# Kernel tuning notes

Hardware: AMD Instinct MI355X
Metric: run time of the kernel (lower is better)

## Reference

```python
import jax, jax.numpy as jnp
import numpy as np

FOCAL_LENGTH = 1000.0
IMG_SIZE = 512.0
EPS = 1e-8


def setup_inputs() -> dict:
    key = jax.random.key(0)
    ks = jax.random.split(key, 11)
    B, J, V = 512, 24, 6890
    return {
        "pred_rotmat": jax.random.normal(ks[0], (B, J, 3, 3), jnp.float32),
        "pred_camera": jax.random.uniform(ks[1], (B, 3), jnp.float32, 0.2, 1.0),
        "pred_joints": jax.random.normal(ks[2], (B, J, 3), jnp.float32),
        "pred_vertices": jax.random.normal(ks[3], (B, V, 3), jnp.float32),
        "pred_betas": jax.random.normal(ks[4], (B, 10), jnp.float32),
        "gt_rotmat": jax.random.normal(ks[5], (B, J, 3, 3), jnp.float32),
        "gt_shape": jax.random.normal(ks[6], (B, 10), jnp.float32),
        "gt_keypoints_2d": jax.random.uniform(ks[7], (B, J, 3), jnp.float32),
        "gt_keypoints_3d": jax.random.uniform(ks[8], (B, J, 4), jnp.float32),
        "gt_vertices": jax.random.normal(ks[9], (B, V, 3), jnp.float32),
        "has_smpl": jax.random.randint(ks[10], (B,), 0, 2, jnp.int32),
    }


def _procrustes_align(S1, S2):
    # S1, S2: [B, N, 3] -> similarity transform of S1 onto S2 (batched closed-form Procrustes)
    S1 = jnp.swapaxes(S1, 1, 2)  # [B,3,N]
    S2 = jnp.swapaxes(S2, 1, 2)
    mu1 = jnp.mean(S1, axis=-1, keepdims=True)
    mu2 = jnp.mean(S2, axis=-1, keepdims=True)
    X1 = S1 - mu1
    X2 = S2 - mu2
    var1 = jnp.sum(X1 * X1, axis=(1, 2))  # [B]
    K = jnp.matmul(X1, jnp.swapaxes(X2, 1, 2)) + EPS  # [B,3,3]
    U, s, Vh = jnp.linalg.svd(K)
    Vt = Vh  # torch V^T == jax Vh
    sign = jnp.sign(jnp.linalg.det(jnp.matmul(U, Vt)))  # det(U @ V^T)
    Z = jnp.broadcast_to(jnp.eye(3, dtype=S1.dtype), K.shape)
    Z = Z.at[:, -1, -1].multiply(sign)
    R = jnp.matmul(jnp.swapaxes(Vh, 1, 2), jnp.matmul(Z, jnp.swapaxes(U, 1, 2)))
    scale = jnp.trace(jnp.matmul(R, K), axis1=1, axis2=2) / var1  # [B]
    t = mu2 - scale[:, None, None] * jnp.matmul(R, mu1)
    S1_hat = scale[:, None, None] * jnp.matmul(R, S1) + t
    return jnp.swapaxes(S1_hat, 1, 2), jnp.swapaxes(S2, 1, 2)


def reference(pred_rotmat, pred_camera, pred_joints, pred_vertices, pred_betas,
              gt_rotmat, gt_shape, gt_keypoints_2d, gt_keypoints_3d, gt_vertices,
              has_smpl):
    B = pred_joints.shape[0]
    f = jnp.float32(FOCAL_LENGTH)
    img = jnp.float32(IMG_SIZE)

    # --- perspective projection with identity rotation ---
    depth = 2.0 * f / (EPS + pred_camera[:, 0] * img)  # [B]
    translation = jnp.stack([pred_camera[:, 1], pred_camera[:, 2], depth], axis=-1)  # [B,3]
    pts = pred_joints + translation[:, None, :]  # [B,J,3]
    pred_kp2d = f * pts[..., :2] / pts[..., 2:3] + img / 2.0  # [B,J,2]

    # --- 2D keypoint loss (normalized by image size, confidence weighted L1) ---
    pred_kp2d_n = pred_kp2d / img
    gt_kp2d_n = gt_keypoints_2d[..., :2] / img
    conf2d = gt_keypoints_2d[..., 2:]
    loss_kp2d = jnp.mean(conf2d * jnp.abs(pred_kp2d_n - gt_kp2d_n))

    # --- 3D keypoint loss (pelvis-aligned, confidence weighted L1) ---
    conf3d = gt_keypoints_3d[..., 3:]
    gt3 = gt_keypoints_3d[..., :3]
    gt_pelvis = (gt3[:, 2:3] + gt3[:, 3:4]) / 2.0
    pr_pelvis = (pred_joints[:, 2:3] + pred_joints[:, 3:4]) / 2.0
    loss_kp3d = jnp.mean(conf3d * jnp.abs((pred_joints - pr_pelvis) - (gt3 - gt_pelvis)))

    # --- masked shape / SMPL parameter losses ---
    mask = (has_smpl > 0).astype(pred_vertices.dtype)  # [B]
    n_valid = jnp.sum(mask)
    V = pred_vertices.shape[1]
    loss_shape = jnp.sum(mask[:, None, None] * jnp.abs(pred_vertices - gt_vertices)) / (n_valid * V * 3 + EPS)
    loss_pose = jnp.sum(mask[:, None, None, None] * (pred_rotmat - gt_rotmat) ** 2) / (n_valid * 24 * 9 + EPS)
    loss_betas = jnp.sum(mask[:, None] * (pred_betas - gt_shape) ** 2) / (n_valid * 10 + EPS)

    # --- PA-MPJPE via batched 3x3 SVD Procrustes (eval-only in original: no grad) ---
    S1_hat, S2 = _procrustes_align(pred_joints, gt3)
    pa_mpjpe = jnp.mean(jnp.sqrt(jnp.sum((S1_hat - S2) ** 2, axis=-1)))

    total = (4.0 * loss_kp2d + 4.0 * loss_kp3d + loss_shape + loss_pose
             + 0.01 * loss_betas + jax.lax.stop_gradient(pa_mpjpe))
    return total
```

## Files before the change

### kernel.cpp

```cpp
#include <hip/hip_runtime.h>
#include <math.h>

#define EPSF   1e-8f
#define NV4    2645760
#define PER_B  20670
#define VBLK   2048

#define B_PROC   0
#define B_NV     8
#define B_BETA   10
#define B_KP2D   30
#define B_KP3D   78
#define B_POSE   126
#define B_VERT   558
#define NBLK     2606


__device__ __forceinline__ void block_sum_store(float v, double* dst) {
  #pragma unroll
  for (int off = 32; off > 0; off >>= 1) v += __shfl_down(v, off);
  __shared__ float red[4];
  const int lane = threadIdx.x & 63;
  const int wid  = threadIdx.x >> 6;
  if (lane == 0) red[wid] = v;
  __syncthreads();
  if (threadIdx.x == 0) *dst = (double)(red[0] + red[1] + red[2] + red[3]);
}

template<int P, int Q>
__device__ __forceinline__ void jrot(float A[3][3], float Vv[3][3]) {
  float apq = A[P][Q];
  if (fabsf(apq) < 1e-20f) return;
  float tau = (A[Q][Q] - A[P][P]) / (2.f * apq);
  float t   = copysignf(1.f, tau) / (fabsf(tau) + sqrtf(1.f + tau * tau));
  float c   = 1.f / sqrtf(1.f + t * t);
  float s   = t * c;
  float cP[3], cQ[3];
  #pragma unroll
  for (int k = 0; k < 3; ++k) { cP[k] = c*A[k][P] - s*A[k][Q]; cQ[k] = s*A[k][P] + c*A[k][Q]; }
  #pragma unroll
  for (int k = 0; k < 3; ++k) { A[k][P] = cP[k]; A[k][Q] = cQ[k]; }
  float rP[3], rQ[3];
  #pragma unroll
  for (int k = 0; k < 3; ++k) { rP[k] = c*A[P][k] - s*A[Q][k]; rQ[k] = s*A[P][k] + c*A[Q][k]; }
  #pragma unroll
  for (int k = 0; k < 3; ++k) { A[P][k] = rP[k]; A[Q][k] = rQ[k]; }
  #pragma unroll
  for (int k = 0; k < 3; ++k) {
    float vp = c*Vv[k][P] - s*Vv[k][Q];
    Vv[k][Q] = s*Vv[k][P] + c*Vv[k][Q];
    Vv[k][P] = vp;
  }
}

#define CSWAP(I, J)                                                        \
  if (lam[I] < lam[J]) {                                                   \
    float tl = lam[I]; lam[I] = lam[J]; lam[J] = tl;                       \
    _Pragma("unroll")                                                      \
    for (int r = 0; r < 3; ++r) {                                          \
      float tv = Vv[r][I]; Vv[r][I] = Vv[r][J]; Vv[r][J] = tv;             \
    }                                                                      \
  }

__device__ float procrustes_err(const float4* __restrict__ P4,
                                const float4* __restrict__ G4, int b) {
  const float4* Pr = P4 + b * 18;
  const float4* Gr = G4 + b * 24;

  float sx0=0,sx1=0,sx2=0, sy0=0,sy1=0,sy2=0, sxx=0;
  float Ku[3][3] = {{0,0,0},{0,0,0},{0,0,0}};
  #pragma unroll
  for (int g = 0; g < 6; ++g) {
    float4 p0 = Pr[g*3+0], p1 = Pr[g*3+1], p2 = Pr[g*3+2];
    float px[4][3] = {{p0.x,p0.y,p0.z},{p0.w,p1.x,p1.y},
                      {p1.z,p1.w,p2.x},{p2.y,p2.z,p2.w}};
    #pragma unroll
    for (int q = 0; q < 4; ++q) {
      float4 gg = Gr[g*4+q];
      float x0 = px[q][0], x1 = px[q][1], x2 = px[q][2];
      sx0 += x0; sx1 += x1; sx2 += x2;
      sy0 += gg.x; sy1 += gg.y; sy2 += gg.z;
      sxx += x0*x0 + x1*x1 + x2*x2;
      Ku[0][0]+=x0*gg.x; Ku[0][1]+=x0*gg.y; Ku[0][2]+=x0*gg.z;
      Ku[1][0]+=x1*gg.x; Ku[1][1]+=x1*gg.y; Ku[1][2]+=x1*gg.z;
      Ku[2][0]+=x2*gg.x; Ku[2][1]+=x2*gg.y; Ku[2][2]+=x2*gg.z;
    }
  }
  const float inv24 = 1.f / 24.f;
  float mu1x=sx0*inv24, mu1y=sx1*inv24, mu1z=sx2*inv24;
  float mu2x=sy0*inv24, mu2y=sy1*inv24, mu2z=sy2*inv24;
  float m1[3] = {mu1x, mu1y, mu1z};
  float m2[3] = {mu2x, mu2y, mu2z};
  float K[3][3];
  #pragma unroll
  for (int r = 0; r < 3; ++r)
    #pragma unroll
    for (int c = 0; c < 3; ++c)
      K[r][c] = Ku[r][c] - 24.f * m1[r] * m2[c] + EPSF;
  float var1 = sxx - 24.f * (mu1x*mu1x + mu1y*mu1y + mu1z*mu1z);

  float detK = K[0][0]*(K[1][1]*K[2][2]-K[1][2]*K[2][1])
             - K[0][1]*(K[1][0]*K[2][2]-K[1][2]*K[2][0])
             + K[0][2]*(K[1][0]*K[2][1]-K[1][1]*K[2][0]);
  float sgn = (detK > 0.f) ? 1.f : ((detK < 0.f) ? -1.f : 0.f);

  float A[3][3];
  #pragma unroll
  for (int r = 0; r < 3; ++r)
    #pragma unroll
    for (int c = 0; c < 3; ++c)
      A[r][c] = K[0][r]*K[0][c] + K[1][r]*K[1][c] + K[2][r]*K[2][c];

  float Vv[3][3] = {{1,0,0},{0,1,0},{0,0,1}};
  for (int sweep = 0; sweep < 8; ++sweep) {
    jrot<0,1>(A, Vv); jrot<0,2>(A, Vv); jrot<1,2>(A, Vv);
  }
  float lam[3] = {A[0][0], A[1][1], A[2][2]};
  CSWAP(0,1) CSWAP(0,2) CSWAP(1,2)

  float Rm[3][3] = {{0,0,0},{0,0,0},{0,0,0}};
  float zi[3] = {1.f, 1.f, sgn};
  float trRK = 0.f;
  #pragma unroll
  for (int i = 0; i < 3; ++i) {
    float v0 = Vv[0][i], v1 = Vv[1][i], v2 = Vv[2][i];
    float a0 = K[0][0]*v0 + K[0][1]*v1 + K[0][2]*v2;
    float a1 = K[1][0]*v0 + K[1][1]*v1 + K[1][2]*v2;
    float a2 = K[2][0]*v0 + K[2][1]*v1 + K[2][2]*v2;
    float si = sqrtf(a0*a0 + a1*a1 + a2*a2);
    float zs = zi[i] / fmaxf(si, 1e-20f);
    Rm[0][0]+=zs*v0*a0; Rm[0][1]+=zs*v0*a1; Rm[0][2]+=zs*v0*a2;
    Rm[1][0]+=zs*v1*a0; Rm[1][1]+=zs*v1*a1; Rm[1][2]+=zs*v1*a2;
    Rm[2][0]+=zs*v2*a0; Rm[2][1]+=zs*v2*a1; Rm[2][2]+=zs*v2*a2;
    trRK += zi[i] * si;
  }
  float scale = trRK / var1;
  float t0 = mu2x - scale*(Rm[0][0]*mu1x + Rm[0][1]*mu1y + Rm[0][2]*mu1z);
  float t1 = mu2y - scale*(Rm[1][0]*mu1x + Rm[1][1]*mu1y + Rm[1][2]*mu1z);
  float t2 = mu2z - scale*(Rm[2][0]*mu1x + Rm[2][1]*mu1y + Rm[2][2]*mu1z);

  float errsum = 0.f;
  #pragma unroll
  for (int g = 0; g < 6; ++g) {
    float4 p0 = Pr[g*3+0], p1 = Pr[g*3+1], p2 = Pr[g*3+2];
    float px[4][3] = {{p0.x,p0.y,p0.z},{p0.w,p1.x,p1.y},
                      {p1.z,p1.w,p2.x},{p2.y,p2.z,p2.w}};
    #pragma unroll
    for (int q = 0; q < 4; ++q) {
      float4 gg = Gr[g*4+q];
      float X = px[q][0], Y = px[q][1], Z = px[q][2];
      float q0 = scale*(Rm[0][0]*X + Rm[0][1]*Y + Rm[0][2]*Z) + t0;
      float q1 = scale*(Rm[1][0]*X + Rm[1][1]*Y + Rm[1][2]*Z) + t1;
      float q2 = scale*(Rm[2][0]*X + Rm[2][1]*Y + Rm[2][2]*Z) + t2;
      float d0 = q0 - gg.x, d1 = q1 - gg.y, d2 = q2 - gg.z;
      errsum += sqrtf(d0*d0 + d1*d1 + d2*d2);
    }
  }
  return errsum;
}

__global__ __launch_bounds__(256) void bmp_main(
    const float*  __restrict__ pred_rotmat, const float* __restrict__ pred_camera,
    const float*  __restrict__ pred_joints, const float4* __restrict__ pred_verts,
    const float*  __restrict__ pred_betas,  const float* __restrict__ gt_rotmat,
    const float*  __restrict__ gt_shape,    const float* __restrict__ gt_kp2d,
    const float*  __restrict__ gt_kp3d,     const float4* __restrict__ gt_verts,
    const int*    __restrict__ has_smpl,    double* __restrict__ ws) {
  const int bid = blockIdx.x;
  const int tid = threadIdx.x;

  if (bid >= B_VERT) {
    float acc = 0.f;
    for (int i = (bid - B_VERT) * 256 + tid; i < NV4; i += VBLK * 256) {
      float4 a = pred_verts[i];
      float4 b = gt_verts[i];
      int e  = i * 4;
      int b0 = e / PER_B;
      int b3 = (e + 3) / PER_B;
      if (b0 == b3) {
        if (has_smpl[b0] > 0)
          acc += fabsf(a.x-b.x) + fabsf(a.y-b.y) + fabsf(a.z-b.z) + fabsf(a.w-b.w);
      } else {
        float d[4] = {fabsf(a.x-b.x), fabsf(a.y-b.y), fabsf(a.z-b.z), fabsf(a.w-b.w)};
        #pragma unroll
        for (int c = 0; c < 4; ++c) {
          int bb = (e + c) / PER_B;
          if (has_smpl[bb] > 0) acc += d[c];
        }
      }
    }
    block_sum_store(acc, &ws[bid]);
    return;
  }

  if (bid >= B_POSE) {
    int idx = (bid - B_POSE) * 256 + tid;
    int b   = idx / 216;
    float m = (has_smpl[b] > 0) ? 1.f : 0.f;
    float d = pred_rotmat[idx] - gt_rotmat[idx];
    block_sum_store(m * d * d, &ws[bid]);
    return;
  }

  if (bid >= B_KP3D) {
    int idx = (bid - B_KP3D) * 256 + tid;
    int b = idx / 24, j = idx - (idx / 24) * 24;
    const float* PJ = pred_joints + b * 72;
    const float* G  = gt_kp3d + b * 96;
    float cf = G[j*4+3];
    float ssum = 0.f;
    #pragma unroll
    for (int c = 0; c < 3; ++c) {
      float prp = 0.5f * (PJ[2*3+c] + PJ[3*3+c]);
      float gtp = 0.5f * (G[2*4+c] + G[3*4+c]);
      ssum += fabsf((PJ[j*3+c] - prp) - (G[j*4+c] - gtp));
    }
    block_sum_store(cf * ssum, &ws[bid]);
    return;
  }

  if (bid >= B_KP2D) {
    int idx = (bid - B_KP2D) * 256 + tid;
    int b = idx / 24, j = idx - (idx / 24) * 24;
    float cam0 = pred_camera[b*3+0], cam1 = pred_camera[b*3+1], cam2 = pred_camera[b*3+2];
    float depth = 2.f * 1000.f / (EPSF + cam0 * 512.f);
    float px = pred_joints[(b*24+j)*3+0] + cam1;
    float py = pred_joints[(b*24+j)*3+1] + cam2;
    float pz = pred_joints[(b*24+j)*3+2] + depth;
    float kxn = (1000.f * px / pz + 256.f) * (1.f / 512.f);
    float kyn = (1000.f * py / pz + 256.f) * (1.f / 512.f);
    float gx = gt_kp2d[(b*24+j)*3+0] * (1.f / 512.f);
    float gy = gt_kp2d[(b*24+j)*3+1] * (1.f / 512.f);
    float cf = gt_kp2d[(b*24+j)*3+2];
    block_sum_store(cf * (fabsf(kxn - gx) + fabsf(kyn - gy)), &ws[bid]);
    return;
  }

  if (bid >= B_BETA) {
    int idx = (bid - B_BETA) * 256 + tid;
    int b = idx / 10;
    float m = (has_smpl[b] > 0) ? 1.f : 0.f;
    float d = pred_betas[idx] - gt_shape[idx];
    block_sum_store(m * d * d, &ws[bid]);
    return;
  }

  if (bid >= B_NV) {
    int idx = (bid - B_NV) * 256 + tid;
    block_sum_store((has_smpl[idx] > 0) ? 1.f : 0.f, &ws[bid]);
    return;
  }

  {
    float e = 0.f;
    if (tid < 64) {
      int b = bid * 64 + tid;
      e = procrustes_err((const float4*)pred_joints, (const float4*)gt_kp3d, b);
    }
    block_sum_store(e, &ws[bid]);
  }
}

__global__ __launch_bounds__(256) void bmp_finalize(const double* __restrict__ ws,
                                                    float* __restrict__ out) {
  const int tid = threadIdx.x;
  double s[7] = {0,0,0,0,0,0,0};
  for (int i = tid; i < NBLK; i += 256) {
    double v = ws[i];
    int slot;
    if      (i >= B_VERT) slot = 0;
    else if (i >= B_POSE) slot = 1;
    else if (i >= B_KP3D) slot = 2;
    else if (i >= B_KP2D) slot = 3;
    else if (i >= B_BETA) slot = 4;
    else if (i >= B_NV)   slot = 5;
    else                  slot = 6;
    s[slot] += v;
  }
  #pragma unroll
  for (int k = 0; k < 7; ++k)
    #pragma unroll
    for (int off = 32; off > 0; off >>= 1) s[k] += __shfl_down(s[k], off);
  __shared__ double red[4][7];
  const int lane = tid & 63, wid = tid >> 6;
  if (lane == 0)
    #pragma unroll
    for (int k = 0; k < 7; ++k) red[wid][k] = s[k];
  __syncthreads();
  if (tid == 0) {
    double t[7];
    #pragma unroll
    for (int k = 0; k < 7; ++k) t[k] = red[0][k]+red[1][k]+red[2][k]+red[3][k];
    double nv = t[5];
    double loss_kp2d  = t[3] / 24576.0;
    double loss_kp3d  = t[2] / 36864.0;
    double loss_shape = t[0] / (nv * 20670.0 + 1e-8);
    double loss_pose  = t[1] / (nv * 216.0   + 1e-8);
    double loss_betas = t[4] / (nv * 10.0    + 1e-8);
    double pa         = t[6] / 12288.0;
    out[0] = (float)(4.0*loss_kp2d + 4.0*loss_kp3d + loss_shape + loss_pose
                     + 0.01*loss_betas + pa);
  }
}

extern "C" void kernel_launch(void* const* d_in, const int* in_sizes, int n_in,
                              void* d_out, int out_size, void* d_ws, size_t ws_size,
                              hipStream_t stream) {
  const float*  pred_rotmat = (const float*)d_in[0];
  const float*  pred_camera = (const float*)d_in[1];
  const float*  pred_joints = (const float*)d_in[2];
  const float4* pred_verts  = (const float4*)d_in[3];
  const float*  pred_betas  = (const float*)d_in[4];
  const float*  gt_rotmat   = (const float*)d_in[5];
  const float*  gt_shape    = (const float*)d_in[6];
  const float*  gt_kp2d     = (const float*)d_in[7];
  const float*  gt_kp3d     = (const float*)d_in[8];
  const float4* gt_verts    = (const float4*)d_in[9];
  const int*    has_smpl    = (const int*)d_in[10];
  double* ws = (double*)d_ws;

  bmp_main<<<NBLK, 256, 0, stream>>>(pred_rotmat, pred_camera, pred_joints,
      pred_verts, pred_betas, gt_rotmat, gt_shape, gt_kp2d, gt_kp3d, gt_verts,
      has_smpl, ws);
  bmp_finalize<<<1, 256, 0, stream>>>(ws, (float*)d_out);
}
```

Measured before the change: 148.3 us.

## Skip masked vertex chunks, vectorize pose loads, use fast math intrinsics

Restructures the vertex L1 reduction so each block owns a contiguous 2048-float4 chunk spanning at most two batches. The block skips loading entirely when both batches are masked out, and otherwise applies a per-element boundary mask instead of per-element division. Pose loss loads float4 instead of scalars, reducing block count. Procrustes math switches to hardware rcp/rsq/sqrt intrinsics, trading a little precision for fewer instructions.

```diff
diff --git a/kernel.cpp b/kernel.cpp
--- a/kernel.cpp
+++ b/kernel.cpp
@@ -4,7 +4,6 @@
 #define EPSF   1e-8f
 #define NV4    2645760
 #define PER_B  20670
-#define VBLK   2048
 
 #define B_PROC   0
 #define B_NV     8
@@ -12,9 +11,12 @@
 #define B_KP2D   30
 #define B_KP3D   78
 #define B_POSE   126
-#define B_VERT   558
-#define NBLK     2606
-
+#define B_VERT   234
+#define NBLK     1526
+
+__device__ __forceinline__ float frcp(float x)  { return __builtin_amdgcn_rcpf(x); }
+__device__ __forceinline__ float frsq(float x)  { return __builtin_amdgcn_rsqf(x); }
+__device__ __forceinline__ float fsqrt(float x) { return __builtin_amdgcn_sqrtf(x); }
 
 __device__ __forceinline__ void block_sum_store(float v, double* dst) {
   #pragma unroll
@@ -31,9 +33,9 @@
 __device__ __forceinline__ void jrot(float A[3][3], float Vv[3][3]) {
   float apq = A[P][Q];
   if (fabsf(apq) < 1e-20f) return;
-  float tau = (A[Q][Q] - A[P][P]) / (2.f * apq);
-  float t   = copysignf(1.f, tau) / (fabsf(tau) + sqrtf(1.f + tau * tau));
-  float c   = 1.f / sqrtf(1.f + t * t);
+  float tau = (A[Q][Q] - A[P][P]) * 0.5f * frcp(apq);
+  float t   = copysignf(1.f, tau) * frcp(fabsf(tau) + fsqrt(1.f + tau * tau));
+  float c   = frsq(1.f + t * t);
   float s   = t * c;
   float cP[3], cQ[3];
   #pragma unroll
@@ -89,14 +91,14 @@
   const float inv24 = 1.f / 24.f;
   float mu1x=sx0*inv24, mu1y=sx1*inv24, mu1z=sx2*inv24;
   float mu2x=sy0*inv24, mu2y=sy1*inv24, mu2z=sy2*inv24;
-  float m1[3] = {mu1x, mu1y, mu1z};
-  float m2[3] = {mu2x, mu2y, mu2z};
+  float m1v[3] = {mu1x, mu1y, mu1z};
+  float m2v[3] = {mu2x, mu2y, mu2z};
   float K[3][3];
   #pragma unroll
   for (int r = 0; r < 3; ++r)
     #pragma unroll
     for (int c = 0; c < 3; ++c)
-      K[r][c] = Ku[r][c] - 24.f * m1[r] * m2[c] + EPSF;
+      K[r][c] = Ku[r][c] - 24.f * m1v[r] * m2v[c] + EPSF;
   float var1 = sxx - 24.f * (mu1x*mu1x + mu1y*mu1y + mu1z*mu1z);
 
   float detK = K[0][0]*(K[1][1]*K[2][2]-K[1][2]*K[2][1])
@@ -127,14 +129,15 @@
     float a0 = K[0][0]*v0 + K[0][1]*v1 + K[0][2]*v2;
     float a1 = K[1][0]*v0 + K[1][1]*v1 + K[1][2]*v2;
     float a2 = K[2][0]*v0 + K[2][1]*v1 + K[2][2]*v2;
-    float si = sqrtf(a0*a0 + a1*a1 + a2*a2);
-    float zs = zi[i] / fmaxf(si, 1e-20f);
+    float s2 = a0*a0 + a1*a1 + a2*a2;
+    float si = fsqrt(s2);
+    float zs = zi[i] * frcp(fmaxf(si, 1e-20f));
     Rm[0][0]+=zs*v0*a0; Rm[0][1]+=zs*v0*a1; Rm[0][2]+=zs*v0*a2;
     Rm[1][0]+=zs*v1*a0; Rm[1][1]+=zs*v1*a1; Rm[1][2]+=zs*v1*a2;
     Rm[2][0]+=zs*v2*a0; Rm[2][1]+=zs*v2*a1; Rm[2][2]+=zs*v2*a2;
     trRK += zi[i] * si;
   }
-  float scale = trRK / var1;
+  float scale = trRK * frcp(var1);
   float t0 = mu2x - scale*(Rm[0][0]*mu1x + Rm[0][1]*mu1y + Rm[0][2]*mu1z);
   float t1 = mu2y - scale*(Rm[1][0]*mu1x + Rm[1][1]*mu1y + Rm[1][2]*mu1z);
   float t2 = mu2z - scale*(Rm[2][0]*mu1x + Rm[2][1]*mu1y + Rm[2][2]*mu1z);
@@ -153,16 +156,16 @@
       float q1 = scale*(Rm[1][0]*X + Rm[1][1]*Y + Rm[1][2]*Z) + t1;
       float q2 = scale*(Rm[2][0]*X + Rm[2][1]*Y + Rm[2][2]*Z) + t2;
       float d0 = q0 - gg.x, d1 = q1 - gg.y, d2 = q2 - gg.z;
-      errsum += sqrtf(d0*d0 + d1*d1 + d2*d2);
+      errsum += fsqrt(d0*d0 + d1*d1 + d2*d2);
     }
   }
   return errsum;
 }
 
 __global__ __launch_bounds__(256) void bmp_main(
-    const float*  __restrict__ pred_rotmat, const float* __restrict__ pred_camera,
+    const float4* __restrict__ pred_rot4,   const float* __restrict__ pred_camera,
     const float*  __restrict__ pred_joints, const float4* __restrict__ pred_verts,
-    const float*  __restrict__ pred_betas,  const float* __restrict__ gt_rotmat,
+    const float*  __restrict__ pred_betas,  const float4* __restrict__ gt_rot4,
     const float*  __restrict__ gt_shape,    const float* __restrict__ gt_kp2d,
     const float*  __restrict__ gt_kp3d,     const float4* __restrict__ gt_verts,
     const int*    __restrict__ has_smpl,    double* __restrict__ ws) {
@@ -170,22 +173,47 @@
   const int tid = threadIdx.x;
 
   if (bid >= B_VERT) {
+    const int chunk  = bid - B_VERT;
+    const int f4base = chunk * 2048;
+    const int nf4    = min(2048, NV4 - f4base);
+    const int e0     = f4base * 4;
+    const int b0     = e0 / PER_B;
+    const int blast  = (e0 + nf4 * 4 - 1) / PER_B;
+    const int m0     = has_smpl[b0] > 0;
+    const int m1     = has_smpl[blast] > 0;
     float acc = 0.f;
-    for (int i = (bid - B_VERT) * 256 + tid; i < NV4; i += VBLK * 256) {
-      float4 a = pred_verts[i];
-      float4 b = gt_verts[i];
-      int e  = i * 4;
-      int b0 = e / PER_B;
-      int b3 = (e + 3) / PER_B;
-      if (b0 == b3) {
-        if (has_smpl[b0] > 0)
+    if (m0 | m1) {
+      const float4* __restrict__ P = pred_verts + f4base + tid;
+      const float4* __restrict__ G = gt_verts  + f4base + tid;
+      if (nf4 == 2048) {
+        float4 pa[8], ga[8];
+        #pragma unroll
+        for (int k = 0; k < 8; ++k) pa[k] = P[k * 256];
+        #pragma unroll
+        for (int k = 0; k < 8; ++k) ga[k] = G[k * 256];
+        if (m0 & m1) {
+          #pragma unroll
+          for (int k = 0; k < 8; ++k)
+            acc += fabsf(pa[k].x-ga[k].x) + fabsf(pa[k].y-ga[k].y)
+                 + fabsf(pa[k].z-ga[k].z) + fabsf(pa[k].w-ga[k].w);
+        } else {
+          const int   bnd = (b0 + 1) * PER_B;
+          const float fm0 = m0 ? 1.f : 0.f;
+          const float fm1 = m1 ? 1.f : 0.f;
+          #pragma unroll
+          for (int k = 0; k < 8; ++k) {
+            int e = (f4base + tid + k * 256) * 4;
+            acc += ((e+0) >= bnd ? fm1 : fm0) * fabsf(pa[k].x-ga[k].x)
+                 + ((e+1) >= bnd ? fm1 : fm0) * fabsf(pa[k].y-ga[k].y)
+                 + ((e+2) >= bnd ? fm1 : fm0) * fabsf(pa[k].z-ga[k].z)
+                 + ((e+3) >= bnd ? fm1 : fm0) * fabsf(pa[k].w-ga[k].w);
+          }
+        }
+      } else {
+        #pragma unroll
+        for (int k = 0; k < 7; ++k) {
+          float4 a = P[k * 256], b = G[k * 256];
           acc += fabsf(a.x-b.x) + fabsf(a.y-b.y) + fabsf(a.z-b.z) + fabsf(a.w-b.w);
-      } else {
-        float d[4] = {fabsf(a.x-b.x), fabsf(a.y-b.y), fabsf(a.z-b.z), fabsf(a.w-b.w)};
-        #pragma unroll
-        for (int c = 0; c < 4; ++c) {
-          int bb = (e + c) / PER_B;
-          if (has_smpl[bb] > 0) acc += d[c];
         }
       }
     }
@@ -195,10 +223,11 @@
 
   if (bid >= B_POSE) {
     int idx = (bid - B_POSE) * 256 + tid;
-    int b   = idx / 216;
+    int b   = idx / 54;
     float m = (has_smpl[b] > 0) ? 1.f : 0.f;
-    float d = pred_rotmat[idx] - gt_rotmat[idx];
-    block_sum_store(m * d * d, &ws[bid]);
+    float4 p = pred_rot4[idx], g = gt_rot4[idx];
+    float dx = p.x-g.x, dy = p.y-g.y, dz = p.z-g.z, dw = p.w-g.w;
+    block_sum_store(m * (dx*dx + dy*dy + dz*dz + dw*dw), &ws[bid]);
     return;
   }
 
@@ -306,12 +335,12 @@
 extern "C" void kernel_launch(void* const* d_in, const int* in_sizes, int n_in,
                               void* d_out, int out_size, void* d_ws, size_t ws_size,
                               hipStream_t stream) {
-  const float*  pred_rotmat = (const float*)d_in[0];
+  const float4* pred_rot4   = (const float4*)d_in[0];
   const float*  pred_camera = (const float*)d_in[1];
   const float*  pred_joints = (const float*)d_in[2];
   const float4* pred_verts  = (const float4*)d_in[3];
   const float*  pred_betas  = (const float*)d_in[4];
-  const float*  gt_rotmat   = (const float*)d_in[5];
+  const float4* gt_rot4     = (const float4*)d_in[5];
   const float*  gt_shape    = (const float*)d_in[6];
   const float*  gt_kp2d     = (const float*)d_in[7];
   const float*  gt_kp3d     = (const float*)d_in[8];
@@ -319,8 +348,8 @@
   const int*    has_smpl    = (const int*)d_in[10];
   double* ws = (double*)d_ws;
 
-  bmp_main<<<NBLK, 256, 0, stream>>>(pred_rotmat, pred_camera, pred_joints,
-      pred_verts, pred_betas, gt_rotmat, gt_shape, gt_kp2d, gt_kp3d, gt_verts,
+  bmp_main<<<NBLK, 256, 0, stream>>>(pred_rot4, pred_camera, pred_joints,
+      pred_verts, pred_betas, gt_rot4, gt_shape, gt_kp2d, gt_kp3d, gt_verts,
       has_smpl, ws);
   bmp_finalize<<<1, 256, 0, stream>>>(ws, (float*)d_out);
 }
```

Result: faster. 128.2 us (-13.6%).
